# Performance work log

Hardware: AMD Instinct MI355X
Metric: run time of the kernel (lower is better)

The kernel has to match this reference:

```python
import jax, jax.numpy as jnp
import numpy as np

N, T, E, H, V = 32768, 20, 50, 50, 200
PAD = 0

def setup_inputs() -> dict:
    key = jax.random.key(0)
    ks = jax.random.split(key, 11)
    s = 1.0 / np.sqrt(H)  # torch LSTM init scale
    return {
        "char_indices": jax.random.randint(ks[0], (N, T), 0, V, dtype=jnp.int32),
        "word_lengths": jax.random.randint(ks[1], (N,), 0, T + 1, dtype=jnp.int32),
        "emb": jax.random.normal(ks[2], (V, E), jnp.float32) * 0.1,
        "W_ih_f": jax.random.normal(ks[3], (4 * H, E), jnp.float32) * s,
        "W_hh_f": jax.random.normal(ks[4], (4 * H, H), jnp.float32) * s,
        "b_ih_f": jax.random.normal(ks[5], (4 * H,), jnp.float32) * s,
        "b_hh_f": jax.random.normal(ks[6], (4 * H,), jnp.float32) * s,
        "W_ih_b": jax.random.normal(ks[7], (4 * H, E), jnp.float32) * s,
        "W_hh_b": jax.random.normal(ks[8], (4 * H, H), jnp.float32) * s,
        "b_ih_b": jax.random.normal(ks[9], (4 * H,), jnp.float32) * s,
        "b_hh_b": jax.random.normal(ks[10], (4 * H,), jnp.float32) * s,
    }

def _run_dir(x, lengths, W_ih, W_hh, b_ih, b_hh, reverse):
    # x: [N,T,E]; returns final hidden state [N,H] at the word's true boundary.
    n = x.shape[0]
    xg = jnp.einsum('nte,ge->ntg', x, W_ih) + b_ih + b_hh  # [N,T,4H]
    def step(carry, t):
        h, c = carry
        g = xg[:, t] + h @ W_hh.T  # [N,4H]
        i, f, gg, o = jnp.split(g, 4, axis=-1)
        c_new = jax.nn.sigmoid(f) * c + jax.nn.sigmoid(i) * jnp.tanh(gg)
        h_new = jax.nn.sigmoid(o) * jnp.tanh(c_new)
        valid = (t < lengths)[:, None]  # only update inside the word
        return (jnp.where(valid, h_new, h), jnp.where(valid, c_new, c)), None
    ts = jnp.arange(T - 1, -1, -1) if reverse else jnp.arange(T)
    z = jnp.zeros((n, W_hh.shape[1]), x.dtype)
    (h, _), _ = jax.lax.scan(step, (z, z), ts)
    return h

def reference(char_indices, word_lengths, emb, W_ih_f, W_hh_f, b_ih_f, b_hh_f,
              W_ih_b, W_hh_b, b_ih_b, b_hh_b):
    emb = emb.at[PAD].set(0.0)  # padding_idx row is zero
    x = emb[char_indices]  # [N,T,E]
    h_f = _run_dir(x, word_lengths, W_ih_f, W_hh_f, b_ih_f, b_hh_f, reverse=False)
    h_b = _run_dir(x, word_lengths, W_ih_b, W_hh_b, b_ih_b, b_hh_b, reverse=True)
    return jnp.concatenate([h_f, h_b], axis=-1)  # [N, 2H]
```

## Files before the change

### kernel.cpp

```cpp
#include <hip/hip_runtime.h>


#define TT    20
#define HH    50
#define VV    200
#define TILES 13
#define GSTRF 212
#define GS32  (VV * GSTRF)
#define WSH   (TILES * 16 * 64)
#define NW    32768
#define NB_G  50
#define NB_W  104
#define NB_H  128
#define NBLK  4096

#define N2LOG2E (-1.4426950408889634f)
#define P2LOG2E 2.8853900817779268f

typedef __attribute__((ext_vector_type(8))) short bf16x8;
typedef __attribute__((ext_vector_type(4))) float f32x4;

__device__ __forceinline__ float frcp(float x) { return __builtin_amdgcn_rcpf(x); }
#if __has_builtin(__builtin_amdgcn_exp2f)
__device__ __forceinline__ float fexp2(float x) { return __builtin_amdgcn_exp2f(x); }
#else
__device__ __forceinline__ float fexp2(float x) { return exp2f(x); }
#endif

__device__ __forceinline__ short f2bf(float x) {
    unsigned b = __builtin_bit_cast(unsigned, x);
    unsigned r = (b + 0x7FFFu + ((b >> 16) & 1u)) >> 16;
    return (short)r;
}

__global__ void k_prep(const float* __restrict__ emb,
                       const float* __restrict__ Wih_f, const float* __restrict__ bih_f,
                       const float* __restrict__ bhh_f,
                       const float* __restrict__ Wih_b, const float* __restrict__ bih_b,
                       const float* __restrict__ bhh_b,
                       const float* __restrict__ Whh_f, const float* __restrict__ Whh_b,
                       const int* __restrict__ lens,
                       float* __restrict__ G32, short* __restrict__ Wimg,
                       int* __restrict__ cnt) {
    int blk = blockIdx.x;
    int tid = threadIdx.x;
    __shared__ float Wl[4 * HH * HH];
    __shared__ float bs[4 * HH];

    if (blk < NB_G) {
        int d = blk / 25;
        int vbase = (blk % 25) * 8;
        const float* Wih = d ? Wih_b : Wih_f;
        const float* bih = d ? bih_b : bih_f;
        const float* bhh = d ? bhh_b : bhh_f;
        for (int i = tid; i < 4 * HH * HH; i += 256) Wl[i] = Wih[i];
        if (tid < 4 * HH) {
            int g = tid / HH;
            float sc = (g == 2) ? P2LOG2E : N2LOG2E;
            bs[tid] = (bih[tid] + bhh[tid]) * sc;
        }
        __syncthreads();
        int r = tid;
        if (r < 4 * HH) {
            int g = r / HH, u = r % HH;
            float sc = (g == 2) ? P2LOG2E : N2LOG2E;
            #pragma unroll
            for (int vv = 0; vv < 8; ++vv) {
                int v = vbase + vv;
                float s = bs[r];
                if (v != 0) {
                    #pragma unroll 10
                    for (int e = 0; e < HH; ++e)
                        s = fmaf(emb[v * HH + e] * sc, Wl[r * HH + e], s);
                }
                G32[d * GS32 + v * GSTRF + u * 4 + g] = s;
            }
        } else {
            int idx = r - 4 * HH;
            for (int k = idx; k < 8 * 12; k += 56) {
                int v = vbase + k / 12;
                int rem = k % 12;
                int u = HH + rem / 4, g = rem & 3;
                G32[d * GS32 + v * GSTRF + u * 4 + g] = 0.0f;
            }
        }
    } else if (blk < NB_G + NB_W) {
        int idx = (blk - NB_G) * 256 + tid;
        if (idx >= 2 * WSH) return;
        int d = idx / WSH;
        int e = idx % WSH;
        int t = e >> 10, m = (e >> 6) & 15, k = e & 63;
        int u = 4 * t + (m >> 2), g = m & 3;
        const float* Whh = d ? Whh_b : Whh_f;
        float sc = (g == 2) ? P2LOG2E : N2LOG2E;
        float val = (k < HH && u < HH) ? Whh[(g * HH + u) * HH + k] * sc : 0.0f;
        int ksw = (k & 7) | (((k >> 3) ^ (m & 7)) << 3);
        Wimg[d * WSH + (e & ~63) + ksw] = f2bf(val);
    } else {
        int hb = blk - NB_G - NB_W;
        __shared__ int hcnt[21];
        if (tid < 21) hcnt[tid] = 0;
        __syncthreads();
        atomicAdd(&hcnt[lens[hb * 256 + tid]], 1);
        __syncthreads();
        if (tid < 21) cnt[hb * 21 + tid] = hcnt[tid];
    }
}

__global__ void k_scat(const int* __restrict__ lens, const int* __restrict__ cnt,
                       int* __restrict__ perm) {
    __shared__ int lcnt[NB_H * 21];
    __shared__ int part[8][21];
    __shared__ int tot[21];
    __shared__ int cur[21];
    int b = blockIdx.x, t = threadIdx.x;
    for (int i = t; i < NB_H * 21; i += 256) lcnt[i] = cnt[i];
    __syncthreads();
    if (t < 168) {
        int L = t % 21, c = t / 21;
        int s = 0;
        for (int bb = c * 16; bb < c * 16 + 16; ++bb) s += lcnt[bb * 21 + L];
        part[c][L] = s;
    }
    __syncthreads();
    if (t < 21) {
        int a = 0;
        #pragma unroll
        for (int c = 0; c < 8; ++c) a += part[c][t];
        tot[t] = a;
    }
    __syncthreads();
    if (t < 21) {
        int a = 0;
        for (int L2 = 20; L2 > t; --L2) a += tot[L2];
        for (int bb = 0; bb < b; ++bb) a += lcnt[bb * 21 + t];
        cur[t] = a;
    }
    __syncthreads();
    int i = b * 256 + t;
    int pos = atomicAdd(&cur[lens[i]], 1);
    perm[pos] = i;
}

__launch_bounds__(512, 6)
__global__ void k_lstm(const int* __restrict__ chars, const int* __restrict__ lens,
                       const int* __restrict__ perm,
                       const float* __restrict__ G32, const short* __restrict__ Wimg,
                       float* __restrict__ out) {
    __shared__ __align__(16) short hs[2][1024];
    __shared__ unsigned short cs[16 * TT];

    int gb   = blockIdx.x;
    int d    = gb & 1;
    int grp  = gb >> 1;
    int tid  = threadIdx.x;
    int lane = tid & 63;
    int wv   = __builtin_amdgcn_readfirstlane(tid >> 6);
    int quad = lane >> 4;
    int n    = lane & 15;
    int x7   = n & 7;
    int slotbase = grp * 16;

    {
        int4 z = {0, 0, 0, 0};
        if (tid < 256) ((int4*)&hs[0][0])[tid] = z;
    }
    for (int i = tid; i < 16 * TT; i += 512) {
        int w = perm[slotbase + i / TT];
        cs[i] = (unsigned short)(chars[w * TT + i % TT] * GSTRF);
    }

    int word = perm[slotbase + n];
    int L = lens[word];
    int mL = L;
    #pragma unroll
    for (int off = 8; off; off >>= 1) {
        int t2 = __shfl_xor(mL, off);
        mL = mL > t2 ? mL : t2;
    }
    mL = __builtin_amdgcn_readfirstlane(mL);

    int pa0 = quad ^ x7;
    int pa1 = (quad + 4) ^ x7;

    int tA = wv, tB = wv + 8;
    int nt = (wv < 5) ? 2 : 1;
    int uA = 4 * tA + quad;
    int uB = 4 * tB + quad;
    int hidxA = n * 64 + (((uA >> 3) ^ x7) << 3) + (uA & 7);
    int hidxB = n * 64 + (((uB >> 3) ^ x7) << 3) + (uB & 7);

    const short* Wd = Wimg + d * WSH;
    bf16x8 A0a = *(const bf16x8*)(Wd + (tA * 16 + n) * 64 + pa0 * 8);
    bf16x8 A1a = *(const bf16x8*)(Wd + (tA * 16 + n) * 64 + pa1 * 8);
    bf16x8 A0b, A1b;
    if (nt == 2) {
        A0b = *(const bf16x8*)(Wd + (tB * 16 + n) * 64 + pa0 * 8);
        A1b = *(const bf16x8*)(Wd + (tB * 16 + n) * 64 + pa1 * 8);
    }

    const float* Gd = G32 + d * GS32 + quad * 4;
    const unsigned short* cw = cs + n * TT;

    float cstA = 0.0f, hfA = 0.0f, cstB = 0.0f, hfB = 0.0f;

    __syncthreads();

    int off0 = cw[(d && L > 0) ? (L - 1) : 0];
    f32x4 gA = *(const f32x4*)(Gd + off0 + tA * 16);
    f32x4 gB;
    if (nt == 2) gB = *(const f32x4*)(Gd + off0 + tB * 16);
    int cur = 0;

    #pragma unroll 1
    for (int s = 0; s < mL; ++s) {
        bool valid = s < L;

        const short* hb = hs[cur];
        bf16x8 B0 = *(const bf16x8*)(hb + n * 64 + pa0 * 8);
        bf16x8 B1 = *(const bf16x8*)(hb + n * 64 + pa1 * 8);

        int sn = s + 1;
        int pn = (sn < L) ? (d ? (L - 1 - sn) : sn) : 0;
        int offn = cw[pn];

        f32x4 aA = gA;
        aA = __builtin_amdgcn_mfma_f32_16x16x32_bf16(A0a, B0, aA, 0, 0, 0);
        aA = __builtin_amdgcn_mfma_f32_16x16x32_bf16(A1a, B1, aA, 0, 0, 0);
        f32x4 aB;
        if (nt == 2) {
            aB = gB;
            aB = __builtin_amdgcn_mfma_f32_16x16x32_bf16(A0b, B0, aB, 0, 0, 0);
            aB = __builtin_amdgcn_mfma_f32_16x16x32_bf16(A1b, B1, aB, 0, 0, 0);
        }

        gA = *(const f32x4*)(Gd + offn + tA * 16);
        if (nt == 2) gB = *(const f32x4*)(Gd + offn + tB * 16);

        {
            float ig = frcp(1.0f + fexp2(aA[0]));
            float fg = frcp(1.0f + fexp2(aA[1]));
            float tg = 1.0f - 2.0f * frcp(1.0f + fexp2(aA[2]));
            float og = frcp(1.0f + fexp2(aA[3]));
            float cn = fg * cstA + ig * tg;
            float hn = og * (1.0f - 2.0f * frcp(1.0f + fexp2(cn * P2LOG2E)));
            bool upd = valid && (uA < HH);
            cstA = upd ? cn : cstA;
            hfA  = upd ? hn : hfA;
        }
        if (nt == 2) {
            float ig = frcp(1.0f + fexp2(aB[0]));
            float fg = frcp(1.0f + fexp2(aB[1]));
            float tg = 1.0f - 2.0f * frcp(1.0f + fexp2(aB[2]));
            float og = frcp(1.0f + fexp2(aB[3]));
            float cn = fg * cstB + ig * tg;
            float hn = og * (1.0f - 2.0f * frcp(1.0f + fexp2(cn * P2LOG2E)));
            bool upd = valid && (uB < HH);
            cstB = upd ? cn : cstB;
            hfB  = upd ? hn : hfB;
        }

        short* hnb = hs[cur ^ 1];
        if (uA < HH) hnb[hidxA] = f2bf(hfA);
        if (nt == 2 && uB < HH) hnb[hidxB] = f2bf(hfB);
        __syncthreads();
        cur ^= 1;
    }

    float* orow = out + (size_t)word * (2 * HH) + d * HH;
    if (uA < HH) orow[uA] = hfA;
    if (nt == 2 && uB < HH) orow[uB] = hfB;
}

extern "C" void kernel_launch(void* const* d_in, const int* in_sizes, int n_in,
                              void* d_out, int out_size, void* d_ws, size_t ws_size,
                              hipStream_t stream) {
    const int*   chars = (const int*)d_in[0];
    const int*   lens  = (const int*)d_in[1];
    const float* emb   = (const float*)d_in[2];
    const float* Wih_f = (const float*)d_in[3];
    const float* Whh_f = (const float*)d_in[4];
    const float* bih_f = (const float*)d_in[5];
    const float* bhh_f = (const float*)d_in[6];
    const float* Wih_b = (const float*)d_in[7];
    const float* Whh_b = (const float*)d_in[8];
    const float* bih_b = (const float*)d_in[9];
    const float* bhh_b = (const float*)d_in[10];
    float* out = (float*)d_out;

    float* G32 = (float*)d_ws;
    short* Wimg = (short*)(G32 + 2 * GS32);
    int*   cnt  = (int*)(Wimg + 2 * WSH);
    int*   perm = cnt + NB_H * 21;

    k_prep<<<NB_G + NB_W + NB_H, 256, 0, stream>>>(emb, Wih_f, bih_f, bhh_f,
                                                   Wih_b, bih_b, bhh_b,
                                                   Whh_f, Whh_b, lens,
                                                   G32, Wimg, cnt);
    k_scat<<<NB_H, 256, 0, stream>>>(lens, cnt, perm);
    k_lstm<<<NBLK, 512, 0, stream>>>(chars, lens, perm, G32, Wimg, out);
}
```

Baseline: 156.4 us.

## Shrink LSTM blocks to two waves with seven tiles each and bf16 gate table

Each block of the recurrent LSTM kernel now uses 128 threads (2 waves) instead of 512, and each wave handles up to 7 gate tiles of the hidden dimension in a register-resident loop rather than 1-2 tiles. The per-step cost of __syncthreads across 8 waves and the idle waves are meant to go away, at the price of a longer serial chain per wave. The precomputed input-projection table is also stored in bf16 instead of fp32, halving its footprint and load size, with reduced precision in the gate pre-activations. The scale factors are folded into W_ih before the dot product rather than into emb.

```diff
diff --git a/kernel.cpp b/kernel.cpp
--- a/kernel.cpp
+++ b/kernel.cpp
@@ -5,8 +5,8 @@
 #define HH    50
 #define VV    200
 #define TILES 13
-#define GSTRF 212
-#define GS32  (VV * GSTRF)
+#define GSTR  212
+#define GSH   (VV * GSTR)
 #define WSH   (TILES * 16 * 64)
 #define NW    32768
 #define NB_G  50
@@ -31,6 +31,12 @@
     unsigned b = __builtin_bit_cast(unsigned, x);
     unsigned r = (b + 0x7FFFu + ((b >> 16) & 1u)) >> 16;
     return (short)r;
+}
+__device__ __forceinline__ float bfhi(unsigned w) {
+    return __builtin_bit_cast(float, w & 0xFFFF0000u);
+}
+__device__ __forceinline__ float bflo(unsigned w) {
+    return __builtin_bit_cast(float, w << 16);
 }
 
 __global__ void k_prep(const float* __restrict__ emb,
@@ -40,7 +46,7 @@
                        const float* __restrict__ bhh_b,
                        const float* __restrict__ Whh_f, const float* __restrict__ Whh_b,
                        const int* __restrict__ lens,
-                       float* __restrict__ G32, short* __restrict__ Wimg,
+                       short* __restrict__ Gimg, short* __restrict__ Wimg,
                        int* __restrict__ cnt) {
     int blk = blockIdx.x;
     int tid = threadIdx.x;
@@ -53,17 +59,19 @@
         const float* Wih = d ? Wih_b : Wih_f;
         const float* bih = d ? bih_b : bih_f;
         const float* bhh = d ? bhh_b : bhh_f;
-        for (int i = tid; i < 4 * HH * HH; i += 256) Wl[i] = Wih[i];
+        for (int i = tid; i < 4 * HH * HH; i += 256) {
+            int r = i / HH;
+            float sc = (r / HH == 2) ? P2LOG2E : N2LOG2E;
+            Wl[i] = Wih[i] * sc;
+        }
         if (tid < 4 * HH) {
-            int g = tid / HH;
-            float sc = (g == 2) ? P2LOG2E : N2LOG2E;
+            float sc = (tid / HH == 2) ? P2LOG2E : N2LOG2E;
             bs[tid] = (bih[tid] + bhh[tid]) * sc;
         }
         __syncthreads();
         int r = tid;
         if (r < 4 * HH) {
             int g = r / HH, u = r % HH;
-            float sc = (g == 2) ? P2LOG2E : N2LOG2E;
             #pragma unroll
             for (int vv = 0; vv < 8; ++vv) {
                 int v = vbase + vv;
@@ -71,17 +79,14 @@
                 if (v != 0) {
                     #pragma unroll 10
                     for (int e = 0; e < HH; ++e)
-                        s = fmaf(emb[v * HH + e] * sc, Wl[r * HH + e], s);
+                        s = fmaf(emb[v * HH + e], Wl[r * HH + e], s);
                 }
-                G32[d * GS32 + v * GSTRF + u * 4 + g] = s;
+                Gimg[d * GSH + v * GSTR + u * 4 + g] = f2bf(s);
             }
         } else {
-            int idx = r - 4 * HH;
-            for (int k = idx; k < 8 * 12; k += 56) {
+            for (int k = r - 4 * HH; k < 8 * 12; k += 56) {
                 int v = vbase + k / 12;
-                int rem = k % 12;
-                int u = HH + rem / 4, g = rem & 3;
-                G32[d * GS32 + v * GSTRF + u * 4 + g] = 0.0f;
+                Gimg[d * GSH + v * GSTR + 4 * HH + (k % 12)] = 0;
             }
         }
     } else if (blk < NB_G + NB_W) {
@@ -142,10 +147,10 @@
     perm[pos] = i;
 }
 
-__launch_bounds__(512, 6)
+__launch_bounds__(128, 4)
 __global__ void k_lstm(const int* __restrict__ chars, const int* __restrict__ lens,
                        const int* __restrict__ perm,
-                       const float* __restrict__ G32, const short* __restrict__ Wimg,
+                       const short* __restrict__ Gimg, const short* __restrict__ Wimg,
                        float* __restrict__ out) {
     __shared__ __align__(16) short hs[2][1024];
     __shared__ unsigned short cs[16 * TT];
@@ -163,11 +168,13 @@
 
     {
         int4 z = {0, 0, 0, 0};
-        if (tid < 256) ((int4*)&hs[0][0])[tid] = z;
-    }
-    for (int i = tid; i < 16 * TT; i += 512) {
+        int4* hz = (int4*)&hs[0][0];
+        hz[tid] = z;
+        hz[tid + 128] = z;
+    }
+    for (int i = tid; i < 16 * TT; i += 128) {
         int w = perm[slotbase + i / TT];
-        cs[i] = (unsigned short)(chars[w * TT + i % TT] * GSTRF);
+        cs[i] = (unsigned short)(chars[w * TT + i % TT] * GSTR);
     }
 
     int word = perm[slotbase + n];
@@ -182,34 +189,34 @@
 
     int pa0 = quad ^ x7;
     int pa1 = (quad + 4) ^ x7;
-
-    int tA = wv, tB = wv + 8;
-    int nt = (wv < 5) ? 2 : 1;
-    int uA = 4 * tA + quad;
-    int uB = 4 * tB + quad;
-    int hidxA = n * 64 + (((uA >> 3) ^ x7) << 3) + (uA & 7);
-    int hidxB = n * 64 + (((uB >> 3) ^ x7) << 3) + (uB & 7);
+    int tbase = wv * 6;
+    int u0 = 4 * tbase + quad;
 
     const short* Wd = Wimg + d * WSH;
-    bf16x8 A0a = *(const bf16x8*)(Wd + (tA * 16 + n) * 64 + pa0 * 8);
-    bf16x8 A1a = *(const bf16x8*)(Wd + (tA * 16 + n) * 64 + pa1 * 8);
-    bf16x8 A0b, A1b;
-    if (nt == 2) {
-        A0b = *(const bf16x8*)(Wd + (tB * 16 + n) * 64 + pa0 * 8);
-        A1b = *(const bf16x8*)(Wd + (tB * 16 + n) * 64 + pa1 * 8);
-    }
-
-    const float* Gd = G32 + d * GS32 + quad * 4;
+    bf16x8 A0[7], A1[7];
+    #pragma unroll
+    for (int tt = 0; tt < 7; ++tt) {
+        int t = tbase + tt;
+        A0[tt] = *(const bf16x8*)(Wd + (t * 16 + n) * 64 + pa0 * 8);
+        A1[tt] = *(const bf16x8*)(Wd + (t * 16 + n) * 64 + pa1 * 8);
+    }
+    int hidx[7];
+    #pragma unroll
+    for (int tt = 0; tt < 7; ++tt) {
+        int uu = u0 + 4 * tt;
+        hidx[tt] = n * 64 + (((uu >> 3) ^ x7) << 3) + (uu & 7);
+    }
+
+    const short* Gq = Gimg + d * GSH + quad * 4 + tbase * 16;
     const unsigned short* cw = cs + n * TT;
 
-    float cstA = 0.0f, hfA = 0.0f, cstB = 0.0f, hfB = 0.0f;
-
-    __syncthreads();
-
-    int off0 = cw[(d && L > 0) ? (L - 1) : 0];
-    f32x4 gA = *(const f32x4*)(Gd + off0 + tA * 16);
-    f32x4 gB;
-    if (nt == 2) gB = *(const f32x4*)(Gd + off0 + tB * 16);
+    float cst[7], hf[7];
+    #pragma unroll
+    for (int tt = 0; tt < 7; ++tt) { cst[tt] = 0.0f; hf[tt] = 0.0f; }
+
+    __syncthreads();
+
+    int vcur = cw[(d && L > 0) ? (L - 1) : 0];
     int cur = 0;
 
     #pragma unroll 1
@@ -222,54 +229,47 @@
 
         int sn = s + 1;
         int pn = (sn < L) ? (d ? (L - 1 - sn) : sn) : 0;
-        int offn = cw[pn];
-
-        f32x4 aA = gA;
-        aA = __builtin_amdgcn_mfma_f32_16x16x32_bf16(A0a, B0, aA, 0, 0, 0);
-        aA = __builtin_amdgcn_mfma_f32_16x16x32_bf16(A1a, B1, aA, 0, 0, 0);
-        f32x4 aB;
-        if (nt == 2) {
-            aB = gB;
-            aB = __builtin_amdgcn_mfma_f32_16x16x32_bf16(A0b, B0, aB, 0, 0, 0);
-            aB = __builtin_amdgcn_mfma_f32_16x16x32_bf16(A1b, B1, aB, 0, 0, 0);
+        int vnxt = cw[pn];
+
+        const int2* gp = (const int2*)(Gq + vcur);
+        short* hnb = hs[cur ^ 1];
+
+        #pragma unroll
+        for (int tt = 0; tt < 7; ++tt) {
+            int2 gw = gp[tt * 4];
+            f32x4 a;
+            a[0] = bflo((unsigned)gw.x);
+            a[1] = bfhi((unsigned)gw.x);
+            a[2] = bflo((unsigned)gw.y);
+            a[3] = bfhi((unsigned)gw.y);
+            a = __builtin_amdgcn_mfma_f32_16x16x32_bf16(A0[tt], B0, a, 0, 0, 0);
+            a = __builtin_amdgcn_mfma_f32_16x16x32_bf16(A1[tt], B1, a, 0, 0, 0);
+
+            float ig = frcp(1.0f + fexp2(a[0]));
+            float fg = frcp(1.0f + fexp2(a[1]));
+            float tg = 1.0f - 2.0f * frcp(1.0f + fexp2(a[2]));
+            float og = frcp(1.0f + fexp2(a[3]));
+            float cn = fg * cst[tt] + ig * tg;
+            float hn = og * (1.0f - 2.0f * frcp(1.0f + fexp2(cn * P2LOG2E)));
+
+            int uu = u0 + 4 * tt;
+            bool upd = valid && (uu < HH);
+            cst[tt] = upd ? cn : cst[tt];
+            hf[tt]  = upd ? hn : hf[tt];
+            if (uu < HH) hnb[hidx[tt]] = f2bf(hf[tt]);
         }
 
-        gA = *(const f32x4*)(Gd + offn + tA * 16);
-        if (nt == 2) gB = *(const f32x4*)(Gd + offn + tB * 16);
-
-        {
-            float ig = frcp(1.0f + fexp2(aA[0]));
-            float fg = frcp(1.0f + fexp2(aA[1]));
-            float tg = 1.0f - 2.0f * frcp(1.0f + fexp2(aA[2]));
-            float og = frcp(1.0f + fexp2(aA[3]));
-            float cn = fg * cstA + ig * tg;
-            float hn = og * (1.0f - 2.0f * frcp(1.0f + fexp2(cn * P2LOG2E)));
-            bool upd = valid && (uA < HH);
-            cstA = upd ? cn : cstA;
-            hfA  = upd ? hn : hfA;
-        }
-        if (nt == 2) {
-            float ig = frcp(1.0f + fexp2(aB[0]));
-            float fg = frcp(1.0f + fexp2(aB[1]));
-            float tg = 1.0f - 2.0f * frcp(1.0f + fexp2(aB[2]));
-            float og = frcp(1.0f + fexp2(aB[3]));
-            float cn = fg * cstB + ig * tg;
-            float hn = og * (1.0f - 2.0f * frcp(1.0f + fexp2(cn * P2LOG2E)));
-            bool upd = valid && (uB < HH);
-            cstB = upd ? cn : cstB;
-            hfB  = upd ? hn : hfB;
-        }
-
-        short* hnb = hs[cur ^ 1];
-        if (uA < HH) hnb[hidxA] = f2bf(hfA);
-        if (nt == 2 && uB < HH) hnb[hidxB] = f2bf(hfB);
+        vcur = vnxt;
         __syncthreads();
         cur ^= 1;
     }
 
     float* orow = out + (size_t)word * (2 * HH) + d * HH;
-    if (uA < HH) orow[uA] = hfA;
-    if (nt == 2 && uB < HH) orow[uB] = hfB;
+    #pragma unroll
+    for (int tt = 0; tt < 7; ++tt) {
+        int uu = u0 + 4 * tt;
+        if (uu < HH) orow[uu] = hf[tt];
+    }
 }
 
 extern "C" void kernel_launch(void* const* d_in, const int* in_sizes, int n_in,
@@ -288,15 +288,15 @@
     const float* bhh_b = (const float*)d_in[10];
     float* out = (float*)d_out;
 
-    float* G32 = (float*)d_ws;
-    short* Wimg = (short*)(G32 + 2 * GS32);
+    short* Gimg = (short*)d_ws;
+    short* Wimg = Gimg + 2 * GSH;
     int*   cnt  = (int*)(Wimg + 2 * WSH);
     int*   perm = cnt + NB_H * 21;
 
     k_prep<<<NB_G + NB_W + NB_H, 256, 0, stream>>>(emb, Wih_f, bih_f, bhh_f,
                                                    Wih_b, bih_b, bhh_b,
                                                    Whh_f, Whh_b, lens,
-                                                   G32, Wimg, cnt);
+                                                   Gimg, Wimg, cnt);
     k_scat<<<NB_H, 256, 0, stream>>>(lens, cnt, perm);
-    k_lstm<<<NBLK, 512, 0, stream>>>(chars, lens, perm, G32, Wimg, out);
-}
+    k_lstm<<<NBLK, 128, 0, stream>>>(chars, lens, perm, Gimg, Wimg, out);
+}
```

After: 163.9 us. 1.05x slower.
